# Kernel optimization log

Measured on AMD Instinct MI355X. Metric: run time of the kernel, lower is better.

Reference implementation:

```python
import jax, jax.numpy as jnp
import numpy as np

N_NODES = 100000
D_IN = 128
D_OUT = 128
N_EDGES = 50000
EDGE_SIZE = 16  # nodes per hyperedge (assumed unique within an edge)


def setup_inputs() -> dict:
    key = jax.random.key(0)
    ks = jax.random.split(key, 8)
    # hypergraph in flat membership (CSR-like) form
    member_nodes = jax.random.randint(ks[0], (N_EDGES * EDGE_SIZE,), 0, N_NODES)
    edge_ids = jnp.repeat(jnp.arange(N_EDGES), EDGE_SIZE)
    H = jax.random.normal(ks[1], (N_NODES, D_IN), dtype=jnp.float32)
    input_weight = jax.random.uniform(ks[2], (N_NODES, 2), dtype=jnp.float32)
    std = 1.0 / np.sqrt(D_OUT)
    W = jax.random.uniform(ks[3], (D_IN, D_OUT), minval=-std, maxval=std, dtype=jnp.float32)
    bias = jax.random.uniform(ks[4], (D_OUT,), minval=-std, maxval=std, dtype=jnp.float32)

    def lin(k, fan_in, fan_out):
        b = 1.0 / np.sqrt(fan_in)
        k1, k2 = jax.random.split(k)
        w = jax.random.uniform(k1, (fan_in, fan_out), minval=-b, maxval=b, dtype=jnp.float32)
        bb = jax.random.uniform(k2, (fan_out,), minval=-b, maxval=b, dtype=jnp.float32)
        return w, bb

    fc1_w, fc1_b = lin(ks[5], 2, 10)
    fc2_w, fc2_b = lin(ks[6], 10, 5)
    fc3_w, fc3_b = lin(ks[7], 5, 1)
    return {
        "member_nodes": member_nodes, "edge_ids": edge_ids,
        "H": H, "input_weight": input_weight,
        "W": W, "bias": bias,
        "fc1_w": fc1_w, "fc1_b": fc1_b,
        "fc2_w": fc2_w, "fc2_b": fc2_b,
        "fc3_w": fc3_w, "fc3_b": fc3_b,
    }


def reference(member_nodes, edge_ids, H, input_weight, W, bias,
              fc1_w, fc1_b, fc2_w, fc2_b, fc3_w, fc3_b):
    # Weight_net (eval mode -> dropout is identity): per-node scalar weight in (0,1)
    h1 = jax.nn.relu(input_weight @ fc1_w + fc1_b)
    h2 = jax.nn.relu(h1 @ fc2_w + fc2_b)
    W2 = jax.nn.sigmoid(h2 @ fc3_w + fc3_b)  # [N, 1]

    # signal_shift_hypergraph_: per-edge weighted sum, broadcast, scatter-add
    HW2 = H * W2                                   # [N, d]
    gathered = HW2[member_nodes]                   # [M, d]
    edge_sum = jax.ops.segment_sum(gathered, edge_ids, num_segments=N_EDGES)   # [E, d]
    edge_size = jax.ops.segment_sum(jnp.ones((member_nodes.shape[0],), H.dtype),
                                    edge_ids, num_segments=N_EDGES)            # [E]
    contrib = (edge_sum[edge_ids] - H[member_nodes]) / (edge_size[edge_ids] - 1.0)[:, None]
    new_signal = H + jax.ops.segment_sum(contrib, member_nodes, num_segments=N_NODES)

    # row-normalize (1/rowsum with inf -> 0)
    rowsum = new_signal.sum(axis=1)
    r_inv = jnp.where(rowsum != 0, 1.0 / rowsum, 0.0)
    AH = new_signal * r_inv[:, None]

    return AH @ W + bias
```

## Files before the change

kernel.cpp:

```cpp
#include <hip/hip_runtime.h>
#include <math.h>

#define EDGE_SZ 16
#define CAP 32
#define BIN_CAP 2560

typedef __attribute__((ext_vector_type(8))) short bf16x8;
typedef __attribute__((ext_vector_type(4))) float f32x4;

__device__ __forceinline__ unsigned short f2bf(float x) {
    unsigned u = __builtin_bit_cast(unsigned, x);
    unsigned r = (u + 0x7fff + ((u >> 16) & 1)) >> 16;
    return (unsigned short)r;
}
__device__ __forceinline__ unsigned pack2bf(float lo, float hi) {
    return ((unsigned)f2bf(hi) << 16) | (unsigned)f2bf(lo);
}
__device__ __forceinline__ float bf_lo(unsigned u) {
    return __builtin_bit_cast(float, u << 16);
}
__device__ __forceinline__ float bf_hi(unsigned u) {
    return __builtin_bit_cast(float, u & 0xffff0000u);
}

__global__ __launch_bounds__(256) void init_kernel(
    const float* __restrict__ W, unsigned short* __restrict__ Wtg,
    int* __restrict__ binCursor, int nbins)
{
    int i = blockIdx.x * blockDim.x + threadIdx.x;
    if (i < nbins) binCursor[i] = 0;
    if (i < 16384) {
        int nn = i >> 7, k = i & 127;
        Wtg[i] = f2bf(W[k * 128 + nn]);
    }
}

__global__ __launch_bounds__(256) void prep_kernel(
    const float* __restrict__ H, const float* __restrict__ iw,
    const float* __restrict__ fc1_w, const float* __restrict__ fc1_b,
    const float* __restrict__ fc2_w, const float* __restrict__ fc2_b,
    const float* __restrict__ fc3_w, const float* __restrict__ fc3_b,
    unsigned* __restrict__ Hwb, float* __restrict__ Hs, float* __restrict__ Hws,
    int n)
{
    int wave = __builtin_amdgcn_readfirstlane(
        blockIdx.x * (blockDim.x >> 6) + (threadIdx.x >> 6));
    int lane = threadIdx.x & 63;
    if (wave >= n) return;
    float xx = iw[wave * 2 + 0], xy = iw[wave * 2 + 1];
    float h1[10];
#pragma unroll
    for (int j = 0; j < 10; ++j) {
        float v = xx * fc1_w[j] + xy * fc1_w[10 + j] + fc1_b[j];
        h1[j] = v > 0.f ? v : 0.f;
    }
    float h2[5];
#pragma unroll
    for (int j = 0; j < 5; ++j) {
        float v = fc2_b[j];
#pragma unroll
        for (int k = 0; k < 10; ++k) v += h1[k] * fc2_w[k * 5 + j];
        h2[j] = v > 0.f ? v : 0.f;
    }
    float z = fc3_b[0];
#pragma unroll
    for (int j = 0; j < 5; ++j) z += h2[j] * fc3_w[j];
    float w2v = 1.f / (1.f + expf(-z));

    float2 h = ((const float2*)H)[wave * 64 + lane];
    Hwb[wave * 64 + lane] = pack2bf(h.x * w2v, h.y * w2v);
    float part = h.x + h.y;
#pragma unroll
    for (int off = 32; off >= 1; off >>= 1) part += __shfl_xor(part, off, 64);
    if (lane == 0) { Hs[wave] = part; Hws[wave] = part * w2v; }
}

__global__ __launch_bounds__(256) void bin_kernel(
    const int* __restrict__ mn, int* __restrict__ binCursor,
    unsigned* __restrict__ stage, int m)
{
    __shared__ int hist[512];
    __shared__ int base[512];
    int t = threadIdx.x;
    for (int i = t; i < 512; i += 256) hist[i] = 0;
    __syncthreads();
    int start = blockIdx.x * 2048;
    int nodev[8], loff[8];
#pragma unroll
    for (int j = 0; j < 8; ++j) {
        int i = start + j * 256 + t;
        nodev[j] = (i < m) ? mn[i] : -1;
        loff[j] = (nodev[j] >= 0) ? atomicAdd(&hist[nodev[j] >> 8], 1) : 0;
    }
    __syncthreads();
    for (int b = t; b < 512; b += 256)
        base[b] = (hist[b] > 0) ? atomicAdd(&binCursor[b], hist[b]) : 0;
    __syncthreads();
#pragma unroll
    for (int j = 0; j < 8; ++j) {
        if (nodev[j] >= 0) {
            int b = nodev[j] >> 8;
            int pos = base[b] + loff[j];
            int i = start + j * 256 + t;
            if (pos < BIN_CAP)
                stage[b * BIN_CAP + pos] =
                    ((unsigned)(i >> 4) << 8) | (unsigned)(nodev[j] & 255);
        }
    }
}

__global__ __launch_bounds__(256) void bucket_kernel(
    const unsigned* __restrict__ stage, const int* __restrict__ binCursor,
    unsigned short* __restrict__ bucket, int* __restrict__ cursor, int n)
{
    __shared__ __align__(16) unsigned short lb[256 * CAP];
    __shared__ int lc[256];
    int t = threadIdx.x;
    int b = blockIdx.x;
    for (int i = t; i < 4096; i += 256) ((unsigned*)lb)[i] = 0;
    lc[t] = 0;
    __syncthreads();
    int cnt = binCursor[b]; if (cnt > BIN_CAP) cnt = BIN_CAP;
    for (int i = t; i < cnt; i += 256) {
        unsigned u = stage[b * BIN_CAP + i];
        int nloc = u & 255;
        int e = u >> 8;
        int p = atomicAdd(&lc[nloc], 1);
        if (p < CAP) lb[nloc * CAP + p] = (unsigned short)e;
    }
    __syncthreads();
    int nbase = b << 8;
    for (int i = t; i < 1024; i += 256) {
        int nloc = i >> 2;
        int node = nbase + nloc;
        if (node < n)
            ((uint4*)bucket)[(size_t)node * 4 + (i & 3)] = ((const uint4*)lb)[i];
    }
    int node = nbase + t;
    if (node < n) cursor[node] = lc[t];
}

__global__ __launch_bounds__(256) void edge_sum_kernel(
    const int* __restrict__ mn, const unsigned* __restrict__ Hwb,
    const float* __restrict__ Hws, unsigned* __restrict__ esb,
    float* __restrict__ Se, int E)
{
    int pair = __builtin_amdgcn_readfirstlane(
        blockIdx.x * (blockDim.x >> 6) + (threadIdx.x >> 6));
    int lane = threadIdx.x & 63;
    int e0 = pair * 2;
    if (e0 >= E) return;
    int e1 = e0 + 1;
    int n0[EDGE_SZ], n1[EDGE_SZ];
#pragma unroll
    for (int m = 0; m < EDGE_SZ; ++m) n0[m] = mn[e0 * EDGE_SZ + m];
#pragma unroll
    for (int m = 0; m < EDGE_SZ; ++m) n1[m] = mn[e1 * EDGE_SZ + m];
    unsigned u0[EDGE_SZ], u1[EDGE_SZ];
#pragma unroll
    for (int m = 0; m < EDGE_SZ; ++m) u0[m] = Hwb[n0[m] * 64 + lane];
#pragma unroll
    for (int m = 0; m < EDGE_SZ; ++m) u1[m] = Hwb[n1[m] * 64 + lane];
    float se0 = 0.f, se1 = 0.f;
#pragma unroll
    for (int m = 0; m < EDGE_SZ; ++m) { se0 += Hws[n0[m]]; se1 += Hws[n1[m]]; }
    float ax0 = 0.f, ay0 = 0.f, ax1 = 0.f, ay1 = 0.f;
#pragma unroll
    for (int m = 0; m < EDGE_SZ; ++m) {
        ax0 += bf_lo(u0[m]); ay0 += bf_hi(u0[m]);
        ax1 += bf_lo(u1[m]); ay1 += bf_hi(u1[m]);
    }
    esb[e0 * 64 + lane] = pack2bf(ax0, ay0);
    esb[e1 * 64 + lane] = pack2bf(ax1, ay1);
    if (lane == 0) { Se[e0] = se0; Se[e1] = se1; }
}

__global__ __launch_bounds__(256) void node_update_kernel(
    const float* __restrict__ H, const unsigned* __restrict__ esb,
    const float* __restrict__ Hs, const float* __restrict__ Se,
    const int* __restrict__ cursor, const unsigned short* __restrict__ bucket,
    unsigned* __restrict__ AHb, int n, int E)
{
    int grp = __builtin_amdgcn_readfirstlane(
        blockIdx.x * (blockDim.x >> 6) + (threadIdx.x >> 6));
    int lane = threadIdx.x & 63;
    int base = grp * 4;
    if (base >= n) return;
    float2 h[4];
    int d[4];
    const unsigned* bp[4];
    float ax[4], ay[4], ss[4];
    int dm = 0;
#pragma unroll
    for (int q = 0; q < 4; ++q) {
        int nq = base + q; if (nq >= n) nq = n - 1;
        h[q] = ((const float2*)H)[nq * 64 + lane];
        int dq = cursor[nq]; if (dq > CAP) dq = CAP;
        if (base + q >= n) dq = 0;
        d[q] = dq;
        if (dq > dm) dm = dq;
        bp[q] = (const unsigned*)(bucket + (size_t)nq * CAP);
        ax[q] = 0.f; ay[q] = 0.f; ss[q] = 0.f;
    }
    for (int k0 = 0; k0 < dm; k0 += 8) {
        int e[4][8];
#pragma unroll
        for (int q = 0; q < 4; ++q)
#pragma unroll
            for (int j = 0; j < 8; ++j) {
                unsigned dw = bp[q][(k0 >> 1) + (j >> 1)];
                unsigned ev = (j & 1) ? (dw >> 16) : (dw & 0xffffu);
                e[q][j] = ev < (unsigned)E ? (int)ev : 0;
            }
        unsigned v[4][8];
#pragma unroll
        for (int q = 0; q < 4; ++q)
#pragma unroll
            for (int j = 0; j < 8; ++j) v[q][j] = esb[e[q][j] * 64 + lane];
        float s[4][8];
#pragma unroll
        for (int q = 0; q < 4; ++q)
#pragma unroll
            for (int j = 0; j < 8; ++j) s[q][j] = Se[e[q][j]];
#pragma unroll
        for (int q = 0; q < 4; ++q)
#pragma unroll
            for (int j = 0; j < 8; ++j) {
                bool p = (k0 + j < d[q]);
                ax[q] += p ? bf_lo(v[q][j]) : 0.f;
                ay[q] += p ? bf_hi(v[q][j]) : 0.f;
                ss[q] += p ? s[q][j] : 0.f;
            }
    }
    const float inv15 = 1.f / 15.f;
#pragma unroll
    for (int q = 0; q < 4; ++q) {
        if (base + q >= n) break;
        int nq = base + q;
        float sc = 1.f - (float)d[q] * inv15;
        float nx = h[q].x * sc + ax[q] * inv15;
        float ny = h[q].y * sc + ay[q] * inv15;
        float st = Hs[nq] * sc + ss[q] * inv15;
        float ri = (st != 0.f) ? 1.f / st : 0.f;
        AHb[nq * 64 + lane] = pack2bf(nx * ri, ny * ri);
    }
}

#define WT_LD 136
__global__ __launch_bounds__(256) void gemm_kernel(
    const unsigned short* __restrict__ AHb, const unsigned short* __restrict__ Wtg,
    const float* __restrict__ bias, float* __restrict__ out, int M)
{
    __shared__ short Wt[128 * WT_LD];
    int t = threadIdx.x;
    for (int i = t; i < 8192; i += 256) {
        unsigned dw = ((const unsigned*)Wtg)[i];
        int n = i >> 6, k2 = i & 63;
        *(unsigned*)&Wt[n * WT_LD + k2 * 2] = dw;
    }
    __syncthreads();

    int lane = t & 63;
    int m16 = lane & 15;
    int quad = lane >> 4;
    int wrow0 = blockIdx.x * 64 + (t >> 6) * 16;

    int arow = wrow0 + m16;
    if (arow >= M) arow = M - 1;

    f32x4 acc[8] = {};
#pragma unroll
    for (int kc = 0; kc < 4; ++kc) {
        int k0 = kc * 32;
        bf16x8 a = *(const bf16x8*)&AHb[arow * 128 + k0 + quad * 8];
#pragma unroll
        for (int ct = 0; ct < 8; ++ct) {
            bf16x8 b = *(const bf16x8*)&Wt[(ct * 16 + m16) * WT_LD + k0 + quad * 8];
            acc[ct] = __builtin_amdgcn_mfma_f32_16x16x32_bf16(a, b, acc[ct], 0, 0, 0);
        }
    }

#pragma unroll
    for (int ct = 0; ct < 8; ++ct) {
        float bv = bias[ct * 16 + m16];
#pragma unroll
        for (int r = 0; r < 4; ++r) {
            int row = wrow0 + quad * 4 + r;
            if (row < M)
                out[row * 128 + ct * 16 + m16] = acc[ct][r] + bv;
        }
    }
}

extern "C" void kernel_launch(void* const* d_in, const int* in_sizes, int n_in,
                              void* d_out, int out_size, void* d_ws, size_t ws_size,
                              hipStream_t stream)
{
    const int*   mn   = (const int*)d_in[0];
    const float* H    = (const float*)d_in[2];
    const float* iw   = (const float*)d_in[3];
    const float* W    = (const float*)d_in[4];
    const float* bias = (const float*)d_in[5];
    const float* fc1w = (const float*)d_in[6];
    const float* fc1b = (const float*)d_in[7];
    const float* fc2w = (const float*)d_in[8];
    const float* fc2b = (const float*)d_in[9];
    const float* fc3w = (const float*)d_in[10];
    const float* fc3b = (const float*)d_in[11];
    float* out = (float*)d_out;

    const int M = in_sizes[0];
    const int E = M / EDGE_SZ;
    const int N = in_sizes[2] / 128;
    const int nbins = (N + 255) >> 8;

    char* ws = (char*)d_ws;
    size_t off = 0;
    auto alloc = [&](size_t bytes) -> char* {
        char* p = ws + off;
        off = (off + bytes + 15) & ~(size_t)15;
        return p;
    };
    unsigned*       Hwb    = (unsigned*)alloc((size_t)N * 64 * 4);
    float*          Hs     = (float*)alloc((size_t)N * 4);
    float*          Hws    = (float*)alloc((size_t)N * 4);
    unsigned*       esb    = (unsigned*)alloc((size_t)E * 64 * 4);
    float*          Se     = (float*)alloc((size_t)E * 4);
    unsigned*       AHb    = (unsigned*)alloc((size_t)N * 64 * 4);
    int*            cursor = (int*)alloc((size_t)N * 4);
    unsigned short* bucket = (unsigned short*)alloc((size_t)N * CAP * 2);
    unsigned short* Wtg    = (unsigned short*)alloc((size_t)128 * 128 * 2);
    int*            binCur = (int*)alloc((size_t)nbins * 4);
    unsigned*       stage  = (unsigned*)alloc((size_t)nbins * BIN_CAP * 4);
    (void)ws_size;

    init_kernel<<<64, 256, 0, stream>>>(W, Wtg, binCur, nbins);
    bin_kernel<<<(M + 2047) / 2048, 256, 0, stream>>>(mn, binCur, stage, M);
    bucket_kernel<<<nbins, 256, 0, stream>>>(stage, binCur, bucket, cursor, N);
    prep_kernel<<<(N + 3) / 4, 256, 0, stream>>>(
        H, iw, fc1w, fc1b, fc2w, fc2b, fc3w, fc3b, Hwb, Hs, Hws, N);
    edge_sum_kernel<<<(E / 2 + 3) / 4, 256, 0, stream>>>(mn, Hwb, Hws, esb, Se, E);
    node_update_kernel<<<((N + 3) / 4 + 3) / 4, 256, 0, stream>>>(
        H, esb, Hs, Se, cursor, bucket, AHb, N, E);
    gemm_kernel<<<(N + 63) / 64, 256, 0, stream>>>(
        (const unsigned short*)AHb, Wtg, bias, out, N);
}
```

Before: 264.2 us.

## Fuse node update into GEMM and merge bucket and prep kernels

```diff
diff --git a/kernel.cpp b/kernel.cpp
--- a/kernel.cpp
+++ b/kernel.cpp
@@ -4,6 +4,7 @@
 #define EDGE_SZ 16
 #define CAP 32
 #define BIN_CAP 2560
+#define AH_LD 136
 
 typedef __attribute__((ext_vector_type(8))) short bf16x8;
 typedef __attribute__((ext_vector_type(4))) float f32x4;
@@ -33,46 +34,6 @@
         int nn = i >> 7, k = i & 127;
         Wtg[i] = f2bf(W[k * 128 + nn]);
     }
-}
-
-__global__ __launch_bounds__(256) void prep_kernel(
-    const float* __restrict__ H, const float* __restrict__ iw,
-    const float* __restrict__ fc1_w, const float* __restrict__ fc1_b,
-    const float* __restrict__ fc2_w, const float* __restrict__ fc2_b,
-    const float* __restrict__ fc3_w, const float* __restrict__ fc3_b,
-    unsigned* __restrict__ Hwb, float* __restrict__ Hs, float* __restrict__ Hws,
-    int n)
-{
-    int wave = __builtin_amdgcn_readfirstlane(
-        blockIdx.x * (blockDim.x >> 6) + (threadIdx.x >> 6));
-    int lane = threadIdx.x & 63;
-    if (wave >= n) return;
-    float xx = iw[wave * 2 + 0], xy = iw[wave * 2 + 1];
-    float h1[10];
-#pragma unroll
-    for (int j = 0; j < 10; ++j) {
-        float v = xx * fc1_w[j] + xy * fc1_w[10 + j] + fc1_b[j];
-        h1[j] = v > 0.f ? v : 0.f;
-    }
-    float h2[5];
-#pragma unroll
-    for (int j = 0; j < 5; ++j) {
-        float v = fc2_b[j];
-#pragma unroll
-        for (int k = 0; k < 10; ++k) v += h1[k] * fc2_w[k * 5 + j];
-        h2[j] = v > 0.f ? v : 0.f;
-    }
-    float z = fc3_b[0];
-#pragma unroll
-    for (int j = 0; j < 5; ++j) z += h2[j] * fc3_w[j];
-    float w2v = 1.f / (1.f + expf(-z));
-
-    float2 h = ((const float2*)H)[wave * 64 + lane];
-    Hwb[wave * 64 + lane] = pack2bf(h.x * w2v, h.y * w2v);
-    float part = h.x + h.y;
-#pragma unroll
-    for (int off = 32; off >= 1; off >>= 1) part += __shfl_xor(part, off, 64);
-    if (lane == 0) { Hs[wave] = part; Hws[wave] = part * w2v; }
 }
 
 __global__ __launch_bounds__(256) void bin_kernel(
@@ -109,35 +70,74 @@
     }
 }
 
-__global__ __launch_bounds__(256) void bucket_kernel(
+__global__ __launch_bounds__(256) void bucket_prep_kernel(
     const unsigned* __restrict__ stage, const int* __restrict__ binCursor,
-    unsigned short* __restrict__ bucket, int* __restrict__ cursor, int n)
+    unsigned short* __restrict__ bucket, int* __restrict__ cursor,
+    const float* __restrict__ H, const float* __restrict__ iw,
+    const float* __restrict__ fc1_w, const float* __restrict__ fc1_b,
+    const float* __restrict__ fc2_w, const float* __restrict__ fc2_b,
+    const float* __restrict__ fc3_w, const float* __restrict__ fc3_b,
+    unsigned* __restrict__ Hwb, float* __restrict__ Hs, float* __restrict__ Hws,
+    int n, int nbins)
 {
     __shared__ __align__(16) unsigned short lb[256 * CAP];
     __shared__ int lc[256];
     int t = threadIdx.x;
-    int b = blockIdx.x;
-    for (int i = t; i < 4096; i += 256) ((unsigned*)lb)[i] = 0;
-    lc[t] = 0;
-    __syncthreads();
-    int cnt = binCursor[b]; if (cnt > BIN_CAP) cnt = BIN_CAP;
-    for (int i = t; i < cnt; i += 256) {
-        unsigned u = stage[b * BIN_CAP + i];
-        int nloc = u & 255;
-        int e = u >> 8;
-        int p = atomicAdd(&lc[nloc], 1);
-        if (p < CAP) lb[nloc * CAP + p] = (unsigned short)e;
-    }
-    __syncthreads();
-    int nbase = b << 8;
-    for (int i = t; i < 1024; i += 256) {
-        int nloc = i >> 2;
-        int node = nbase + nloc;
-        if (node < n)
-            ((uint4*)bucket)[(size_t)node * 4 + (i & 3)] = ((const uint4*)lb)[i];
-    }
-    int node = nbase + t;
-    if (node < n) cursor[node] = lc[t];
+    if ((int)blockIdx.x < nbins) {
+        int b = blockIdx.x;
+        for (int i = t; i < 4096; i += 256) ((unsigned*)lb)[i] = 0;
+        lc[t] = 0;
+        __syncthreads();
+        int cnt = binCursor[b]; if (cnt > BIN_CAP) cnt = BIN_CAP;
+        for (int i = t; i < cnt; i += 256) {
+            unsigned u = stage[b * BIN_CAP + i];
+            int nloc = u & 255;
+            int e = u >> 8;
+            int p = atomicAdd(&lc[nloc], 1);
+            if (p < CAP) lb[nloc * CAP + p] = (unsigned short)e;
+        }
+        __syncthreads();
+        int nbase = b << 8;
+        for (int i = t; i < 1024; i += 256) {
+            int nloc = i >> 2;
+            int node = nbase + nloc;
+            if (node < n)
+                ((uint4*)bucket)[(size_t)node * 4 + (i & 3)] = ((const uint4*)lb)[i];
+        }
+        int node = nbase + t;
+        if (node < n) cursor[node] = lc[t];
+        return;
+    }
+    int wave = __builtin_amdgcn_readfirstlane(
+        ((int)blockIdx.x - nbins) * (blockDim.x >> 6) + (t >> 6));
+    int lane = t & 63;
+    if (wave >= n) return;
+    float xx = iw[wave * 2 + 0], xy = iw[wave * 2 + 1];
+    float h1[10];
+#pragma unroll
+    for (int j = 0; j < 10; ++j) {
+        float v = xx * fc1_w[j] + xy * fc1_w[10 + j] + fc1_b[j];
+        h1[j] = v > 0.f ? v : 0.f;
+    }
+    float h2[5];
+#pragma unroll
+    for (int j = 0; j < 5; ++j) {
+        float v = fc2_b[j];
+#pragma unroll
+        for (int k = 0; k < 10; ++k) v += h1[k] * fc2_w[k * 5 + j];
+        h2[j] = v > 0.f ? v : 0.f;
+    }
+    float z = fc3_b[0];
+#pragma unroll
+    for (int j = 0; j < 5; ++j) z += h2[j] * fc3_w[j];
+    float w2v = 1.f / (1.f + expf(-z));
+
+    float2 h = ((const float2*)H)[wave * 64 + lane];
+    Hwb[wave * 64 + lane] = pack2bf(h.x * w2v, h.y * w2v);
+    float part = h.x + h.y;
+#pragma unroll
+    for (int off = 32; off >= 1; off >>= 1) part += __shfl_xor(part, off, 64);
+    if (lane == 0) { Hs[wave] = part; Hws[wave] = part * w2v; }
 }
 
 __global__ __launch_bounds__(256) void edge_sum_kernel(
@@ -175,118 +175,104 @@
     if (lane == 0) { Se[e0] = se0; Se[e1] = se1; }
 }
 
-__global__ __launch_bounds__(256) void node_update_kernel(
+__global__ __launch_bounds__(256) void node_gemm_kernel(
     const float* __restrict__ H, const unsigned* __restrict__ esb,
     const float* __restrict__ Hs, const float* __restrict__ Se,
     const int* __restrict__ cursor, const unsigned short* __restrict__ bucket,
-    unsigned* __restrict__ AHb, int n, int E)
-{
-    int grp = __builtin_amdgcn_readfirstlane(
-        blockIdx.x * (blockDim.x >> 6) + (threadIdx.x >> 6));
-    int lane = threadIdx.x & 63;
-    int base = grp * 4;
-    if (base >= n) return;
-    float2 h[4];
-    int d[4];
-    const unsigned* bp[4];
-    float ax[4], ay[4], ss[4];
-    int dm = 0;
-#pragma unroll
-    for (int q = 0; q < 4; ++q) {
-        int nq = base + q; if (nq >= n) nq = n - 1;
-        h[q] = ((const float2*)H)[nq * 64 + lane];
-        int dq = cursor[nq]; if (dq > CAP) dq = CAP;
-        if (base + q >= n) dq = 0;
-        d[q] = dq;
-        if (dq > dm) dm = dq;
-        bp[q] = (const unsigned*)(bucket + (size_t)nq * CAP);
-        ax[q] = 0.f; ay[q] = 0.f; ss[q] = 0.f;
-    }
-    for (int k0 = 0; k0 < dm; k0 += 8) {
-        int e[4][8];
-#pragma unroll
-        for (int q = 0; q < 4; ++q)
-#pragma unroll
-            for (int j = 0; j < 8; ++j) {
-                unsigned dw = bp[q][(k0 >> 1) + (j >> 1)];
-                unsigned ev = (j & 1) ? (dw >> 16) : (dw & 0xffffu);
-                e[q][j] = ev < (unsigned)E ? (int)ev : 0;
-            }
-        unsigned v[4][8];
-#pragma unroll
-        for (int q = 0; q < 4; ++q)
-#pragma unroll
-            for (int j = 0; j < 8; ++j) v[q][j] = esb[e[q][j] * 64 + lane];
-        float s[4][8];
-#pragma unroll
-        for (int q = 0; q < 4; ++q)
-#pragma unroll
-            for (int j = 0; j < 8; ++j) s[q][j] = Se[e[q][j]];
-#pragma unroll
-        for (int q = 0; q < 4; ++q)
-#pragma unroll
-            for (int j = 0; j < 8; ++j) {
-                bool p = (k0 + j < d[q]);
-                ax[q] += p ? bf_lo(v[q][j]) : 0.f;
-                ay[q] += p ? bf_hi(v[q][j]) : 0.f;
-                ss[q] += p ? s[q][j] : 0.f;
-            }
-    }
+    const unsigned short* __restrict__ Wtg, const float* __restrict__ bias,
+    float* __restrict__ out, int n, int E)
+{
+    __shared__ __align__(16) short AH[64 * AH_LD];
+    int t = threadIdx.x;
+    int w = t >> 6;
+    int lane = t & 63;
+    int nodeBase = blockIdx.x * 64 + w * 16;
     const float inv15 = 1.f / 15.f;
-#pragma unroll
-    for (int q = 0; q < 4; ++q) {
-        if (base + q >= n) break;
-        int nq = base + q;
-        float sc = 1.f - (float)d[q] * inv15;
-        float nx = h[q].x * sc + ax[q] * inv15;
-        float ny = h[q].y * sc + ay[q] * inv15;
-        float st = Hs[nq] * sc + ss[q] * inv15;
-        float ri = (st != 0.f) ? 1.f / st : 0.f;
-        AHb[nq * 64 + lane] = pack2bf(nx * ri, ny * ri);
-    }
-}
-
-#define WT_LD 136
-__global__ __launch_bounds__(256) void gemm_kernel(
-    const unsigned short* __restrict__ AHb, const unsigned short* __restrict__ Wtg,
-    const float* __restrict__ bias, float* __restrict__ out, int M)
-{
-    __shared__ short Wt[128 * WT_LD];
-    int t = threadIdx.x;
-    for (int i = t; i < 8192; i += 256) {
-        unsigned dw = ((const unsigned*)Wtg)[i];
-        int n = i >> 6, k2 = i & 63;
-        *(unsigned*)&Wt[n * WT_LD + k2 * 2] = dw;
+
+    for (int g = 0; g < 4; ++g) {
+        int base = nodeBase + g * 4;
+        float2 h[4];
+        int d[4];
+        const unsigned* bp[4];
+        float ax[4], ay[4], ss[4];
+        int dm = 0;
+#pragma unroll
+        for (int q = 0; q < 4; ++q) {
+            int nq = base + q; if (nq >= n) nq = n - 1;
+            h[q] = ((const float2*)H)[nq * 64 + lane];
+            int dq = cursor[nq]; if (dq > CAP) dq = CAP;
+            if (base + q >= n) dq = 0;
+            d[q] = dq;
+            if (dq > dm) dm = dq;
+            bp[q] = (const unsigned*)(bucket + (size_t)nq * CAP);
+            ax[q] = 0.f; ay[q] = 0.f; ss[q] = 0.f;
+        }
+        for (int k0 = 0; k0 < dm; k0 += 8) {
+            int e[4][8];
+#pragma unroll
+            for (int q = 0; q < 4; ++q)
+#pragma unroll
+                for (int j = 0; j < 8; ++j) {
+                    unsigned dw = bp[q][(k0 >> 1) + (j >> 1)];
+                    unsigned ev = (j & 1) ? (dw >> 16) : (dw & 0xffffu);
+                    e[q][j] = ev < (unsigned)E ? (int)ev : 0;
+                }
+            unsigned v[4][8];
+#pragma unroll
+            for (int q = 0; q < 4; ++q)
+#pragma unroll
+                for (int j = 0; j < 8; ++j) v[q][j] = esb[e[q][j] * 64 + lane];
+            float s[4][8];
+#pragma unroll
+            for (int q = 0; q < 4; ++q)
+#pragma unroll
+                for (int j = 0; j < 8; ++j) s[q][j] = Se[e[q][j]];
+#pragma unroll
+            for (int q = 0; q < 4; ++q)
+#pragma unroll
+                for (int j = 0; j < 8; ++j) {
+                    bool p = (k0 + j < d[q]);
+                    ax[q] += p ? bf_lo(v[q][j]) : 0.f;
+                    ay[q] += p ? bf_hi(v[q][j]) : 0.f;
+                    ss[q] += p ? s[q][j] : 0.f;
+                }
+        }
+#pragma unroll
+        for (int q = 0; q < 4; ++q) {
+            int nq = base + q; if (nq >= n) nq = n - 1;
+            float sc = 1.f - (float)d[q] * inv15;
+            float nx = h[q].x * sc + ax[q] * inv15;
+            float ny = h[q].y * sc + ay[q] * inv15;
+            float st = Hs[nq] * sc + ss[q] * inv15;
+            float ri = (st != 0.f) ? 1.f / st : 0.f;
+            *(unsigned*)&AH[(w * 16 + g * 4 + q) * AH_LD + lane * 2] =
+                pack2bf(nx * ri, ny * ri);
+        }
     }
     __syncthreads();
 
-    int lane = t & 63;
     int m16 = lane & 15;
     int quad = lane >> 4;
-    int wrow0 = blockIdx.x * 64 + (t >> 6) * 16;
-
-    int arow = wrow0 + m16;
-    if (arow >= M) arow = M - 1;
-
+    int rowl = w * 16 + m16;
     f32x4 acc[8] = {};
 #pragma unroll
     for (int kc = 0; kc < 4; ++kc) {
         int k0 = kc * 32;
-        bf16x8 a = *(const bf16x8*)&AHb[arow * 128 + k0 + quad * 8];
+        bf16x8 a = *(const bf16x8*)&AH[rowl * AH_LD + k0 + quad * 8];
 #pragma unroll
         for (int ct = 0; ct < 8; ++ct) {
-            bf16x8 b = *(const bf16x8*)&Wt[(ct * 16 + m16) * WT_LD + k0 + quad * 8];
+            bf16x8 b = *(const bf16x8*)&Wtg[(ct * 16 + m16) * 128 + k0 + quad * 8];
             acc[ct] = __builtin_amdgcn_mfma_f32_16x16x32_bf16(a, b, acc[ct], 0, 0, 0);
         }
     }
-
+    int wrow0 = blockIdx.x * 64 + w * 16;
 #pragma unroll
     for (int ct = 0; ct < 8; ++ct) {
         float bv = bias[ct * 16 + m16];
 #pragma unroll
         for (int r = 0; r < 4; ++r) {
             int row = wrow0 + quad * 4 + r;
-            if (row < M)
+            if (row < n)
                 out[row * 128 + ct * 16 + m16] = acc[ct][r] + bv;
         }
     }
@@ -326,7 +312,6 @@
     float*          Hws    = (float*)alloc((size_t)N * 4);
     unsigned*       esb    = (unsigned*)alloc((size_t)E * 64 * 4);
     float*          Se     = (float*)alloc((size_t)E * 4);
-    unsigned*       AHb    = (unsigned*)alloc((size_t)N * 64 * 4);
     int*            cursor = (int*)alloc((size_t)N * 4);
     unsigned short* bucket = (unsigned short*)alloc((size_t)N * CAP * 2);
     unsigned short* Wtg    = (unsigned short*)alloc((size_t)128 * 128 * 2);
@@ -334,14 +319,14 @@
     unsigned*       stage  = (unsigned*)alloc((size_t)nbins * BIN_CAP * 4);
     (void)ws_size;
 
+    const int prep_blocks = (N + 3) / 4;
+
     init_kernel<<<64, 256, 0, stream>>>(W, Wtg, binCur, nbins);
     bin_kernel<<<(M + 2047) / 2048, 256, 0, stream>>>(mn, binCur, stage, M);
-    bucket_kernel<<<nbins, 256, 0, stream>>>(stage, binCur, bucket, cursor, N);
-    prep_kernel<<<(N + 3) / 4, 256, 0, stream>>>(
-        H, iw, fc1w, fc1b, fc2w, fc2b, fc3w, fc3b, Hwb, Hs, Hws, N);
+    bucket_prep_kernel<<<nbins + prep_blocks, 256, 0, stream>>>(
+        stage, binCur, bucket, cursor,
+        H, iw, fc1w, fc1b, fc2w, fc2b, fc3w, fc3b, Hwb, Hs, Hws, N, nbins);
     edge_sum_kernel<<<(E / 2 + 3) / 4, 256, 0, stream>>>(mn, Hwb, Hws, esb, Se, E);
-    node_update_kernel<<<((N + 3) / 4 + 3) / 4, 256, 0, stream>>>(
-        H, esb, Hs, Se, cursor, bucket, AHb, N, E);
-    gemm_kernel<<<(N + 63) / 64, 256, 0, stream>>>(
-        (const unsigned short*)AHb, Wtg, bias, out, N);
-}
+    node_gemm_kernel<<<(N + 63) / 64, 256, 0, stream>>>(
+        H, esb, Hs, Se, cursor, bucket, Wtg, bias, out, N, E);
+}
```

Result: slower. 327.0 us (+23.8%).

## Merge bucket and prep kernels; use zero sentinel edge to drop masking

Applied to the files above, without the earlier changes.

```diff
diff --git a/kernel.cpp b/kernel.cpp
--- a/kernel.cpp
+++ b/kernel.cpp
@@ -25,54 +25,17 @@
 
 __global__ __launch_bounds__(256) void init_kernel(
     const float* __restrict__ W, unsigned short* __restrict__ Wtg,
-    int* __restrict__ binCursor, int nbins)
+    int* __restrict__ binCursor, int nbins,
+    unsigned* __restrict__ esbSent, float* __restrict__ SeSent)
 {
     int i = blockIdx.x * blockDim.x + threadIdx.x;
     if (i < nbins) binCursor[i] = 0;
+    if (i < 64) esbSent[i] = 0u;
+    if (i == 64) *SeSent = 0.f;
     if (i < 16384) {
         int nn = i >> 7, k = i & 127;
         Wtg[i] = f2bf(W[k * 128 + nn]);
     }
-}
-
-__global__ __launch_bounds__(256) void prep_kernel(
-    const float* __restrict__ H, const float* __restrict__ iw,
-    const float* __restrict__ fc1_w, const float* __restrict__ fc1_b,
-    const float* __restrict__ fc2_w, const float* __restrict__ fc2_b,
-    const float* __restrict__ fc3_w, const float* __restrict__ fc3_b,
-    unsigned* __restrict__ Hwb, float* __restrict__ Hs, float* __restrict__ Hws,
-    int n)
-{
-    int wave = __builtin_amdgcn_readfirstlane(
-        blockIdx.x * (blockDim.x >> 6) + (threadIdx.x >> 6));
-    int lane = threadIdx.x & 63;
-    if (wave >= n) return;
-    float xx = iw[wave * 2 + 0], xy = iw[wave * 2 + 1];
-    float h1[10];
-#pragma unroll
-    for (int j = 0; j < 10; ++j) {
-        float v = xx * fc1_w[j] + xy * fc1_w[10 + j] + fc1_b[j];
-        h1[j] = v > 0.f ? v : 0.f;
-    }
-    float h2[5];
-#pragma unroll
-    for (int j = 0; j < 5; ++j) {
-        float v = fc2_b[j];
-#pragma unroll
-        for (int k = 0; k < 10; ++k) v += h1[k] * fc2_w[k * 5 + j];
-        h2[j] = v > 0.f ? v : 0.f;
-    }
-    float z = fc3_b[0];
-#pragma unroll
-    for (int j = 0; j < 5; ++j) z += h2[j] * fc3_w[j];
-    float w2v = 1.f / (1.f + expf(-z));
-
-    float2 h = ((const float2*)H)[wave * 64 + lane];
-    Hwb[wave * 64 + lane] = pack2bf(h.x * w2v, h.y * w2v);
-    float part = h.x + h.y;
-#pragma unroll
-    for (int off = 32; off >= 1; off >>= 1) part += __shfl_xor(part, off, 64);
-    if (lane == 0) { Hs[wave] = part; Hws[wave] = part * w2v; }
 }
 
 __global__ __launch_bounds__(256) void bin_kernel(
@@ -109,35 +72,75 @@
     }
 }
 
-__global__ __launch_bounds__(256) void bucket_kernel(
+__global__ __launch_bounds__(256) void bucket_prep_kernel(
     const unsigned* __restrict__ stage, const int* __restrict__ binCursor,
-    unsigned short* __restrict__ bucket, int* __restrict__ cursor, int n)
+    unsigned short* __restrict__ bucket, int* __restrict__ cursor,
+    const float* __restrict__ H, const float* __restrict__ iw,
+    const float* __restrict__ fc1_w, const float* __restrict__ fc1_b,
+    const float* __restrict__ fc2_w, const float* __restrict__ fc2_b,
+    const float* __restrict__ fc3_w, const float* __restrict__ fc3_b,
+    unsigned* __restrict__ Hwb, float* __restrict__ Hs, float* __restrict__ Hws,
+    int n, int nbins, int E)
 {
     __shared__ __align__(16) unsigned short lb[256 * CAP];
     __shared__ int lc[256];
     int t = threadIdx.x;
-    int b = blockIdx.x;
-    for (int i = t; i < 4096; i += 256) ((unsigned*)lb)[i] = 0;
-    lc[t] = 0;
-    __syncthreads();
-    int cnt = binCursor[b]; if (cnt > BIN_CAP) cnt = BIN_CAP;
-    for (int i = t; i < cnt; i += 256) {
-        unsigned u = stage[b * BIN_CAP + i];
-        int nloc = u & 255;
-        int e = u >> 8;
-        int p = atomicAdd(&lc[nloc], 1);
-        if (p < CAP) lb[nloc * CAP + p] = (unsigned short)e;
-    }
-    __syncthreads();
-    int nbase = b << 8;
-    for (int i = t; i < 1024; i += 256) {
-        int nloc = i >> 2;
-        int node = nbase + nloc;
-        if (node < n)
-            ((uint4*)bucket)[(size_t)node * 4 + (i & 3)] = ((const uint4*)lb)[i];
-    }
-    int node = nbase + t;
-    if (node < n) cursor[node] = lc[t];
+    if ((int)blockIdx.x < nbins) {
+        int b = blockIdx.x;
+        unsigned sent = (unsigned)E * 0x10001u;
+        for (int i = t; i < 4096; i += 256) ((unsigned*)lb)[i] = sent;
+        lc[t] = 0;
+        __syncthreads();
+        int cnt = binCursor[b]; if (cnt > BIN_CAP) cnt = BIN_CAP;
+        for (int i = t; i < cnt; i += 256) {
+            unsigned u = stage[b * BIN_CAP + i];
+            int nloc = u & 255;
+            int e = u >> 8;
+            int p = atomicAdd(&lc[nloc], 1);
+            if (p < CAP) lb[nloc * CAP + p] = (unsigned short)e;
+        }
+        __syncthreads();
+        int nbase = b << 8;
+        for (int i = t; i < 1024; i += 256) {
+            int nloc = i >> 2;
+            int node = nbase + nloc;
+            if (node < n)
+                ((uint4*)bucket)[(size_t)node * 4 + (i & 3)] = ((const uint4*)lb)[i];
+        }
+        int node = nbase + t;
+        if (node < n) cursor[node] = lc[t];
+        return;
+    }
+    int wave = __builtin_amdgcn_readfirstlane(
+        ((int)blockIdx.x - nbins) * (blockDim.x >> 6) + (t >> 6));
+    int lane = t & 63;
+    if (wave >= n) return;
+    float xx = iw[wave * 2 + 0], xy = iw[wave * 2 + 1];
+    float h1[10];
+#pragma unroll
+    for (int j = 0; j < 10; ++j) {
+        float v = xx * fc1_w[j] + xy * fc1_w[10 + j] + fc1_b[j];
+        h1[j] = v > 0.f ? v : 0.f;
+    }
+    float h2[5];
+#pragma unroll
+    for (int j = 0; j < 5; ++j) {
+        float v = fc2_b[j];
+#pragma unroll
+        for (int k = 0; k < 10; ++k) v += h1[k] * fc2_w[k * 5 + j];
+        h2[j] = v > 0.f ? v : 0.f;
+    }
+    float z = fc3_b[0];
+#pragma unroll
+    for (int j = 0; j < 5; ++j) z += h2[j] * fc3_w[j];
+    float w2v = 1.f / (1.f + expf(-z));
+
+    float2 h = ((const float2*)H)[wave * 64 + lane];
+    Hwb[wave * 64 + lane] = pack2bf(h.x * w2v, h.y * w2v);
+    float part = h.x + h.y;
+#pragma unroll
+    for (int off = 32; off >= 1; off >>= 1) part += __shfl_xor(part, off, 64);
+    if (lane == 0) { Hs[wave] = part; Hws[wave] = part * w2v; }
 }
 
 __global__ __launch_bounds__(256) void edge_sum_kernel(
@@ -203,33 +206,31 @@
         ax[q] = 0.f; ay[q] = 0.f; ss[q] = 0.f;
     }
     for (int k0 = 0; k0 < dm; k0 += 8) {
-        int e[4][8];
+        unsigned ev[4][8];
 #pragma unroll
         for (int q = 0; q < 4; ++q)
 #pragma unroll
             for (int j = 0; j < 8; ++j) {
                 unsigned dw = bp[q][(k0 >> 1) + (j >> 1)];
-                unsigned ev = (j & 1) ? (dw >> 16) : (dw & 0xffffu);
-                e[q][j] = ev < (unsigned)E ? (int)ev : 0;
+                ev[q][j] = (j & 1) ? (dw >> 16) : (dw & 0xffffu);
             }
         unsigned v[4][8];
 #pragma unroll
         for (int q = 0; q < 4; ++q)
 #pragma unroll
-            for (int j = 0; j < 8; ++j) v[q][j] = esb[e[q][j] * 64 + lane];
+            for (int j = 0; j < 8; ++j) v[q][j] = esb[ev[q][j] * 64 + lane];
         float s[4][8];
 #pragma unroll
         for (int q = 0; q < 4; ++q)
 #pragma unroll
-            for (int j = 0; j < 8; ++j) s[q][j] = Se[e[q][j]];
+            for (int j = 0; j < 8; ++j) s[q][j] = Se[ev[q][j]];
 #pragma unroll
         for (int q = 0; q < 4; ++q)
 #pragma unroll
             for (int j = 0; j < 8; ++j) {
-                bool p = (k0 + j < d[q]);
-                ax[q] += p ? bf_lo(v[q][j]) : 0.f;
-                ay[q] += p ? bf_hi(v[q][j]) : 0.f;
-                ss[q] += p ? s[q][j] : 0.f;
+                ax[q] += bf_lo(v[q][j]);
+                ay[q] += bf_hi(v[q][j]);
+                ss[q] += s[q][j];
             }
     }
     const float inv15 = 1.f / 15.f;
@@ -324,8 +325,8 @@
     unsigned*       Hwb    = (unsigned*)alloc((size_t)N * 64 * 4);
     float*          Hs     = (float*)alloc((size_t)N * 4);
     float*          Hws    = (float*)alloc((size_t)N * 4);
-    unsigned*       esb    = (unsigned*)alloc((size_t)E * 64 * 4);
-    float*          Se     = (float*)alloc((size_t)E * 4);
+    unsigned*       esb    = (unsigned*)alloc((size_t)(E + 1) * 64 * 4);
+    float*          Se     = (float*)alloc((size_t)(E + 1) * 4);
     unsigned*       AHb    = (unsigned*)alloc((size_t)N * 64 * 4);
     int*            cursor = (int*)alloc((size_t)N * 4);
     unsigned short* bucket = (unsigned short*)alloc((size_t)N * CAP * 2);
@@ -334,11 +335,14 @@
     unsigned*       stage  = (unsigned*)alloc((size_t)nbins * BIN_CAP * 4);
     (void)ws_size;
 
-    init_kernel<<<64, 256, 0, stream>>>(W, Wtg, binCur, nbins);
+    const int prep_blocks = (N + 3) / 4;
+
+    init_kernel<<<64, 256, 0, stream>>>(W, Wtg, binCur, nbins,
+                                        esb + (size_t)E * 64, Se + E);
     bin_kernel<<<(M + 2047) / 2048, 256, 0, stream>>>(mn, binCur, stage, M);
-    bucket_kernel<<<nbins, 256, 0, stream>>>(stage, binCur, bucket, cursor, N);
-    prep_kernel<<<(N + 3) / 4, 256, 0, stream>>>(
-        H, iw, fc1w, fc1b, fc2w, fc2b, fc3w, fc3b, Hwb, Hs, Hws, N);
+    bucket_prep_kernel<<<nbins + prep_blocks, 256, 0, stream>>>(
+        stage, binCur, bucket, cursor,
+        H, iw, fc1w, fc1b, fc2w, fc2b, fc3w, fc3b, Hwb, Hs, Hws, N, nbins, E);
     edge_sum_kernel<<<(E / 2 + 3) / 4, 256, 0, stream>>>(mn, Hwb, Hws, esb, Se, E);
     node_update_kernel<<<((N + 3) / 4 + 3) / 4, 256, 0, stream>>>(
         H, esb, Hs, Se, cursor, bucket, AHb, N, E);
```

Result: faster. 249.3 us (-5.6%).
